# Optimization experiments

Measured on AMD Instinct MI355X. Metric: run time of the kernel, lower is better.

The kernel has to match this reference:

```python
import jax, jax.numpy as jnp
import numpy as np

B, T, N = 128, 32, 196
E = 1024   # embed dim
FD = 1024  # feature dim
H = 1024   # hidden size
A = 1024   # attention dim
SCALE = 0.02


def setup_inputs() -> dict:
    key = jax.random.key(0)
    ks = jax.random.split(key, 16)
    g = lambda k, shape: (jax.random.normal(k, shape, dtype=jnp.float32) * SCALE)
    return {
        "feats": jax.random.normal(ks[0], (B, N, FD), dtype=jnp.float32),
        "embeddings": jax.random.normal(ks[1], (B, T, E), dtype=jnp.float32),
        # additive attention params: v^T tanh(feats @ Wf + h @ Wh + b_att)
        "Wf": g(ks[2], (FD, A)),
        "Wh": g(ks[3], (H, A)),
        "b_att": jnp.zeros((A,), dtype=jnp.float32),
        "v": g(ks[4], (A,)),
        # layer-0 LSTMCell (input = concat(embed, attn) of size E+FD)
        "W_ih0": g(ks[5], (4 * H, E + FD)),
        "W_hh0": g(ks[6], (4 * H, H)),
        "b_ih0": jnp.zeros((4 * H,), dtype=jnp.float32),
        "b_hh0": jnp.zeros((4 * H,), dtype=jnp.float32),
        # layer-1 LSTMCell (input size H)
        "W_ih1": g(ks[7], (4 * H, H)),
        "W_hh1": g(ks[8], (4 * H, H)),
        "b_ih1": jnp.zeros((4 * H,), dtype=jnp.float32),
        "b_hh1": jnp.zeros((4 * H,), dtype=jnp.float32),
    }


def _lstm_cell(x, h, c, W_ih, W_hh, b_ih, b_hh):
    # PyTorch LSTMCell: gates ordered i, f, g, o
    gates = x @ W_ih.T + h @ W_hh.T + (b_ih + b_hh)
    i, f, g, o = jnp.split(gates, 4, axis=-1)
    c_new = jax.nn.sigmoid(f) * c + jax.nn.sigmoid(i) * jnp.tanh(g)
    h_new = jax.nn.sigmoid(o) * jnp.tanh(c_new)
    return h_new, c_new


def reference(feats, embeddings, Wf, Wh, b_att, v, W_ih0, W_hh0, b_ih0, b_hh0,
              W_ih1, W_hh1, b_ih1, b_hh1):
    Bb = embeddings.shape[0]
    # precompute the h-independent half of the attention energies: [B, N, A]
    f_proj = jnp.einsum("bnf,fa->bna", feats, Wf) + b_att

    h0 = jnp.zeros((Bb, H), dtype=feats.dtype)
    c0 = jnp.zeros((Bb, H), dtype=feats.dtype)

    def step(carry, embed_t):
        h0, c0 = carry
        # additive attention with query h0
        e = jnp.tanh(f_proj + (h0 @ Wh)[:, None, :])      # [B, N, A]
        scores = jnp.einsum("bna,a->bn", e, v)            # [B, N]
        alpha = jax.nn.softmax(scores, axis=-1)
        attn = jnp.einsum("bn,bnf->bf", alpha, feats)     # [B, FD]
        x = jnp.concatenate([embed_t, attn], axis=1)      # [B, E+FD]
        h0n, c0n = _lstm_cell(x, h0, c0, W_ih0, W_hh0, b_ih0, b_hh0)
        # faithful to source: layer 1 uses (h0n, c0n) as its state AND h0n as input
        h1, c1 = _lstm_cell(h0n, h0n, c0n, W_ih1, W_hh1, b_ih1, b_hh1)
        return (h0n, c0n), h1

    (_, _), outs = jax.lax.scan(step, (h0, c0), jnp.swapaxes(embeddings, 0, 1))
    return jnp.swapaxes(outs, 0, 1)  # [B, T, H]
```

## Files before the change

kernel.cpp:

```cpp
#include <hip/hip_runtime.h>
#include <cstddef>

typedef unsigned short ushort_t;
typedef unsigned int uint_t;
typedef __attribute__((ext_vector_type(8))) short bf16x8;
typedef __attribute__((ext_vector_type(4))) float f32x4;

constexpr int kB  = 128;
constexpr int kT  = 32;
constexpr int kN  = 196;
constexpr int kH  = 1024;

__device__ __forceinline__ float fsigmoid(float x) { return 1.f / (1.f + __expf(-x)); }
__device__ __forceinline__ float ftanh(float x)    { return 1.f - 2.f / (__expf(2.f * x) + 1.f); }
__device__ __forceinline__ ushort_t f2bf(float f) {
    uint_t u = __float_as_uint(f);
    return (ushort_t)((u + 0x7fffu + ((u >> 16) & 1u)) >> 16);
}

__global__ __launch_bounds__(256) void wf_transpose(
    const float* __restrict__ Wsrc, ushort_t* __restrict__ dst)
{
    __shared__ float t[64][65];
    const int k0 = blockIdx.x * 64, a0 = blockIdx.y * 64;
    const int c = threadIdx.x & 15, r0 = threadIdx.x >> 4;
#pragma unroll
    for (int i = 0; i < 4; ++i) {
        const int r = r0 + i * 16;
        const float4 v = *(const float4*)(Wsrc + (size_t)(k0 + r) * 1024 + a0 + c * 4);
        t[r][c * 4 + 0] = v.x; t[r][c * 4 + 1] = v.y;
        t[r][c * 4 + 2] = v.z; t[r][c * 4 + 3] = v.w;
    }
    __syncthreads();
#pragma unroll
    for (int i = 0; i < 4; ++i) {
        const int r = r0 + i * 16;
        ushort4 h;
        h.x = f2bf(t[c * 4 + 0][r]); h.y = f2bf(t[c * 4 + 1][r]);
        h.z = f2bf(t[c * 4 + 2][r]); h.w = f2bf(t[c * 4 + 3][r]);
        *(ushort4*)&dst[(size_t)(a0 + r) * 1024 + k0 + c * 4] = h;
    }
}

__global__ __launch_bounds__(256) void pack_whh0(
    const float* __restrict__ Whh0, ushort_t* __restrict__ Wbig)
{
    const int idx = blockIdx.x * 256 + threadIdx.x;
    const int j = idx >> 8, k4 = (idx & 255) * 4;
    const int u = j >> 2, g = j & 3;
    const float4 v = *(const float4*)(Whh0 + (size_t)(g * 1024 + u) * 1024 + k4);
    ushort4 h;
    h.x = f2bf(v.x); h.y = f2bf(v.y); h.z = f2bf(v.z); h.w = f2bf(v.w);
    *(ushort4*)&Wbig[(size_t)(1024 + j) * 1024 + k4] = h;
}

__global__ __launch_bounds__(256) void pack_w1sum(
    const float* __restrict__ Wih1, const float* __restrict__ Whh1,
    ushort_t* __restrict__ Wbig)
{
    const int idx = blockIdx.x * 256 + threadIdx.x;
    const int j = idx >> 8, k4 = (idx & 255) * 4;
    const int u = j >> 2, g = j & 3;
    const size_t o = (size_t)(g * 1024 + u) * 1024 + k4;
    const float4 a = *(const float4*)(Wih1 + o);
    const float4 b = *(const float4*)(Whh1 + o);
    ushort4 h;
    h.x = f2bf(a.x + b.x); h.y = f2bf(a.y + b.y);
    h.z = f2bf(a.z + b.z); h.w = f2bf(a.w + b.w);
    *(ushort4*)&Wbig[(size_t)(5120 + j) * 1024 + k4] = h;
}

__global__ __launch_bounds__(256) void pack_w0cat(
    const float* __restrict__ Wih0, ushort_t* __restrict__ W0cat)
{
    const int idx = blockIdx.x * 256 + threadIdx.x;
    const int j = idx >> 9, k4 = (idx & 511) * 4;
    const int u = j >> 2, g = j & 3;
    const int srccol = (k4 < 1024) ? (k4 + 1024) : (k4 - 1024);
    const float4 v = *(const float4*)(Wih0 + (size_t)(g * 1024 + u) * 2048 + srccol);
    ushort4 h;
    h.x = f2bf(v.x); h.y = f2bf(v.y); h.z = f2bf(v.z); h.w = f2bf(v.w);
    *(ushort4*)&W0cat[(size_t)j * 2048 + k4] = h;
}

__global__ __launch_bounds__(256) void cast_bf(
    const float* __restrict__ src, ushort_t* __restrict__ dst)
{
    const size_t idx = ((size_t)blockIdx.x * 256 + threadIdx.x) * 4;
    const float4 v = *(const float4*)(src + idx);
    ushort4 h;
    h.x = f2bf(v.x); h.y = f2bf(v.y); h.z = f2bf(v.z); h.w = f2bf(v.w);
    *(ushort4*)&dst[idx] = h;
}

__global__ __launch_bounds__(256) void fproj_mfma(
    const float* __restrict__ feats, const ushort_t* __restrict__ WfT,
    const float* __restrict__ bias, ushort_t* __restrict__ fprojbf)
{
    __shared__ ushort_t As[128 * 40];
    __shared__ ushort_t Bs[128 * 40];

    const int tid = threadIdx.x;
    const int m0 = blockIdx.x * 128, n0 = blockIdx.y * 128;
    const int lane = tid & 63, w = tid >> 6;
    const int wm = (w & 1) * 64, wn = (w >> 1) * 64;
    const int lr = lane & 15, quad = lane >> 4;

    f32x4 acc[4][4];
#pragma unroll
    for (int i = 0; i < 4; ++i)
#pragma unroll
        for (int j = 0; j < 4; ++j)
            acc[i][j] = (f32x4){0.f, 0.f, 0.f, 0.f};

    for (int k0 = 0; k0 < 1024; k0 += 32) {
#pragma unroll
        for (int it = 0; it < 4; ++it) {
            const int q = it * 256 + tid;
            const int row = q >> 3, kc = (q & 7) * 4;
            const float4 v = *(const float4*)(feats + (size_t)(m0 + row) * 1024 + k0 + kc);
            ushort4 h;
            h.x = f2bf(v.x); h.y = f2bf(v.y); h.z = f2bf(v.z); h.w = f2bf(v.w);
            *(ushort4*)&As[row * 40 + kc] = h;
        }
#pragma unroll
        for (int it = 0; it < 2; ++it) {
            const int q = it * 256 + tid;
            const int row = q >> 2, kc = (q & 3) * 8;
            const uint4 v = *(const uint4*)(WfT + (size_t)(n0 + row) * 1024 + k0 + kc);
            *(uint4*)&Bs[row * 40 + kc] = v;
        }
        __syncthreads();

        bf16x8 af[4], bb[4];
#pragma unroll
        for (int mf = 0; mf < 4; ++mf)
            af[mf] = *(const bf16x8*)&As[(wm + mf * 16 + lr) * 40 + quad * 8];
#pragma unroll
        for (int nf = 0; nf < 4; ++nf)
            bb[nf] = *(const bf16x8*)&Bs[(wn + nf * 16 + lr) * 40 + quad * 8];
#pragma unroll
        for (int mf = 0; mf < 4; ++mf)
#pragma unroll
            for (int nf = 0; nf < 4; ++nf)
                acc[mf][nf] = __builtin_amdgcn_mfma_f32_16x16x32_bf16(
                    af[mf], bb[nf], acc[mf][nf], 0, 0, 0);
        __syncthreads();
    }

#pragma unroll
    for (int nf = 0; nf < 4; ++nf) {
        const int n = n0 + wn + nf * 16 + lr;
        const float bn = bias[n];
#pragma unroll
        for (int mf = 0; mf < 4; ++mf) {
#pragma unroll
            for (int r = 0; r < 4; ++r) {
                const int m = m0 + wm + mf * 16 + quad * 4 + r;
                fprojbf[(size_t)m * 1024 + n] = f2bf(acc[mf][nf][r] + bn);
            }
        }
    }
}

__global__ __launch_bounds__(256) void hgemm_A(
    const ushort_t* __restrict__ hbf, const ushort_t* __restrict__ Wbig,
    const float* __restrict__ cbuf,
    const float* __restrict__ bih1, const float* __restrict__ bhh1,
    float* __restrict__ hwh, float* __restrict__ Ypart,
    float* __restrict__ out, int tstep)
{
    __shared__ ushort_t xs[128 * 40];
    __shared__ ushort_t wsB[64 * 40];
    __shared__ float eps[128][65];

    const int tid = threadIdx.x;
    const int n0 = blockIdx.x * 64;
    const int lane = tid & 63, w = tid >> 6;
    const int wm = (w & 1) * 64, wn = (w >> 1) * 32;
    const int lr = lane & 15, quad = lane >> 4;

    f32x4 acc[4][2];
#pragma unroll
    for (int i = 0; i < 4; ++i) {
        acc[i][0] = (f32x4){0.f, 0.f, 0.f, 0.f};
        acc[i][1] = (f32x4){0.f, 0.f, 0.f, 0.f};
    }

    for (int k0 = 0; k0 < 1024; k0 += 32) {
#pragma unroll
        for (int it = 0; it < 2; ++it) {
            const int q = it * 256 + tid;
            const int row = q >> 2, kc = (q & 3) * 8;
            *(uint4*)&xs[row * 40 + kc] =
                *(const uint4*)&hbf[(size_t)row * 1024 + k0 + kc];
        }
        {
            const int row = tid >> 2, kc = (tid & 3) * 8;
            *(uint4*)&wsB[row * 40 + kc] =
                *(const uint4*)&Wbig[(size_t)(n0 + row) * 1024 + k0 + kc];
        }
        __syncthreads();
        bf16x8 af[4], bb[2];
#pragma unroll
        for (int mf = 0; mf < 4; ++mf)
            af[mf] = *(const bf16x8*)&xs[(wm + mf * 16 + lr) * 40 + quad * 8];
#pragma unroll
        for (int nf = 0; nf < 2; ++nf)
            bb[nf] = *(const bf16x8*)&wsB[(wn + nf * 16 + lr) * 40 + quad * 8];
#pragma unroll
        for (int mf = 0; mf < 4; ++mf)
#pragma unroll
            for (int nf = 0; nf < 2; ++nf)
                acc[mf][nf] = __builtin_amdgcn_mfma_f32_16x16x32_bf16(
                    af[mf], bb[nf], acc[mf][nf], 0, 0, 0);
        __syncthreads();
    }

    if (n0 < 5120) {
        float* dst = (n0 < 1024) ? hwh : Ypart;
        const int stride = (n0 < 1024) ? 1024 : 4096;
        const int nbase = (n0 < 1024) ? n0 : (n0 - 1024);
#pragma unroll
        for (int mf = 0; mf < 4; ++mf)
#pragma unroll
            for (int nf = 0; nf < 2; ++nf)
#pragma unroll
                for (int r = 0; r < 4; ++r) {
                    const int m = wm + mf * 16 + quad * 4 + r;
                    const int n = nbase + wn + nf * 16 + lr;
                    dst[(size_t)m * stride + n] = acc[mf][nf][r];
                }
    } else {
#pragma unroll
        for (int mf = 0; mf < 4; ++mf)
#pragma unroll
            for (int nf = 0; nf < 2; ++nf)
#pragma unroll
                for (int r = 0; r < 4; ++r)
                    eps[wm + mf * 16 + quad * 4 + r][wn + nf * 16 + lr] = acc[mf][nf][r];
        __syncthreads();
        if (tstep >= 1) {
#pragma unroll
            for (int i = 0; i < 8; ++i) {
                const int cid = i * 256 + tid;
                const int b = cid & 127, ulc = cid >> 7;
                const int u = ((n0 - 5120) >> 2) + ulc;
                const float iv = fsigmoid(eps[b][ulc * 4 + 0] + bih1[u]        + bhh1[u]);
                const float fv = fsigmoid(eps[b][ulc * 4 + 1] + bih1[1024 + u] + bhh1[1024 + u]);
                const float gv = ftanh   (eps[b][ulc * 4 + 2] + bih1[2048 + u] + bhh1[2048 + u]);
                const float ov = fsigmoid(eps[b][ulc * 4 + 3] + bih1[3072 + u] + bhh1[3072 + u]);
                const float cp = cbuf[(size_t)b * 1024 + u];
                const float cn = fv * cp + iv * gv;
                out[((size_t)b * kT + (tstep - 1)) * 1024 + u] = ov * ftanh(cn);
            }
        }
    }
}

__global__ __launch_bounds__(256) void scores_kernel(
    const ushort_t* __restrict__ fprojbf, const float* __restrict__ hwh,
    const float* __restrict__ vvec, float* __restrict__ scoresbuf)
{
    const int b = blockIdx.x, chunk = blockIdx.y;
    const int tid = threadIdx.x, lane = tid & 63, w = tid >> 6;

    float hw[16], vr[16];
    {
        const int a0 = lane * 16;
#pragma unroll
        for (int q = 0; q < 4; ++q) {
            const float4 s0 = *(const float4*)(hwh + (size_t)b * 1024 + a0 + q * 4);
            hw[q * 4 + 0] = s0.x; hw[q * 4 + 1] = s0.y;
            hw[q * 4 + 2] = s0.z; hw[q * 4 + 3] = s0.w;
            const float4 vv = *(const float4*)(vvec + a0 + q * 4);
            vr[q * 4 + 0] = vv.x; vr[q * 4 + 1] = vv.y;
            vr[q * 4 + 2] = vv.z; vr[q * 4 + 3] = vv.w;
        }
    }

#pragma unroll
    for (int i = 0; i < 7; ++i) {
        const int n = chunk * 28 + w * 7 + i;
        const ushort_t* fp = fprojbf + ((size_t)(b * kN + n)) * 1024 + lane * 16;
        const uint4 u0 = *(const uint4*)(fp);
        const uint4 u1 = *(const uint4*)(fp + 8);
        float p = 0.f;
        const uint_t uu[8] = {u0.x, u0.y, u0.z, u0.w, u1.x, u1.y, u1.z, u1.w};
#pragma unroll
        for (int q = 0; q < 8; ++q) {
            const float xa = __uint_as_float(uu[q] << 16);
            const float xb = __uint_as_float(uu[q] & 0xffff0000u);
            p += ftanh(xa + hw[2 * q]) * vr[2 * q];
            p += ftanh(xb + hw[2 * q + 1]) * vr[2 * q + 1];
        }
#pragma unroll
        for (int off = 32; off; off >>= 1) p += __shfl_down(p, off);
        if (lane == 0) scoresbuf[b * kN + n] = p;
    }
}

template<int BF>
__global__ __launch_bounds__(256) void attn_kernel(
    const float* __restrict__ scoresbuf, const float* __restrict__ featsf,
    const ushort_t* __restrict__ featsbf, ushort_t* __restrict__ attnbf)
{
    __shared__ float alpha_s[200];
    __shared__ float red[8];
    const int b = blockIdx.x;
    const int tid = threadIdx.x;

    const float val = (tid < kN) ? scoresbuf[b * kN + tid] : -1e30f;
    float m = val;
#pragma unroll
    for (int off = 32; off; off >>= 1) m = fmaxf(m, __shfl_down(m, off));
    if ((tid & 63) == 0) red[tid >> 6] = m;
    __syncthreads();
    m = fmaxf(fmaxf(red[0], red[1]), fmaxf(red[2], red[3]));
    const float e = (tid < kN) ? __expf(val - m) : 0.f;
    float s = e;
#pragma unroll
    for (int off = 32; off; off >>= 1) s += __shfl_down(s, off);
    if ((tid & 63) == 0) red[4 + (tid >> 6)] = s;
    __syncthreads();
    s = red[4] + red[5] + red[6] + red[7];
    if (tid < kN) alpha_s[tid] = e * (1.f / s);
    __syncthreads();

    if (BF) {
        const int f0 = blockIdx.y * 512 + tid * 2;
        const ushort_t* fb = featsbf + (size_t)b * kN * 1024 + f0;
        float a0 = 0.f, a1 = 0.f;
#pragma unroll 4
        for (int n = 0; n < kN; ++n) {
            const uint_t u = *(const uint_t*)(fb + (size_t)n * 1024);
            a0 += alpha_s[n] * __uint_as_float(u << 16);
            a1 += alpha_s[n] * __uint_as_float(u & 0xffff0000u);
        }
        uint_t o = ((uint_t)f2bf(a1) << 16) | (uint_t)f2bf(a0);
        *(uint_t*)&attnbf[(size_t)b * 1024 + f0] = o;
    } else {
        const int f = blockIdx.y * 256 + tid;
        const float* fb = featsf + (size_t)b * kN * 1024 + f;
        float a = 0.f;
#pragma unroll 4
        for (int n = 0; n < kN; ++n) a += alpha_s[n] * fb[(size_t)n * 1024];
        attnbf[(size_t)b * 1024 + f] = f2bf(a);
    }
}

__global__ __launch_bounds__(256) void gatesC(
    const ushort_t* __restrict__ attnbf, const ushort_t* __restrict__ embbf,
    const ushort_t* __restrict__ W0cat, const float* __restrict__ Ypart,
    const float* __restrict__ bih0, const float* __restrict__ bhh0,
    float* __restrict__ cbuf, ushort_t* __restrict__ hbf, int tstep)
{
    __shared__ ushort_t xs[128 * 40];
    __shared__ ushort_t wsB[64 * 40];
    __shared__ float eps[128][65];

    const int tid = threadIdx.x;
    const int n0 = blockIdx.x * 64;
    const int lane = tid & 63, w = tid >> 6;
    const int wm = (w & 1) * 64, wn = (w >> 1) * 32;
    const int lr = lane & 15, quad = lane >> 4;

    f32x4 acc[4][2];
#pragma unroll
    for (int i = 0; i < 4; ++i) {
        acc[i][0] = (f32x4){0.f, 0.f, 0.f, 0.f};
        acc[i][1] = (f32x4){0.f, 0.f, 0.f, 0.f};
    }

    for (int k0 = 0; k0 < 2048; k0 += 32) {
#pragma unroll
        for (int it = 0; it < 2; ++it) {
            const int q = it * 256 + tid;
            const int row = q >> 2, kc = (q & 3) * 8;
            const ushort_t* src = (k0 < 1024)
                ? (attnbf + (size_t)row * 1024 + k0 + kc)
                : (embbf + ((size_t)row * kT + tstep) * 1024 + (k0 - 1024) + kc);
            *(uint4*)&xs[row * 40 + kc] = *(const uint4*)src;
        }
        {
            const int row = tid >> 2, kc = (tid & 3) * 8;
            *(uint4*)&wsB[row * 40 + kc] =
                *(const uint4*)&W0cat[(size_t)(n0 + row) * 2048 + k0 + kc];
        }
        __syncthreads();
        bf16x8 af[4], bb[2];
#pragma unroll
        for (int mf = 0; mf < 4; ++mf)
            af[mf] = *(const bf16x8*)&xs[(wm + mf * 16 + lr) * 40 + quad * 8];
#pragma unroll
        for (int nf = 0; nf < 2; ++nf)
            bb[nf] = *(const bf16x8*)&wsB[(wn + nf * 16 + lr) * 40 + quad * 8];
#pragma unroll
        for (int mf = 0; mf < 4; ++mf)
#pragma unroll
            for (int nf = 0; nf < 2; ++nf)
                acc[mf][nf] = __builtin_amdgcn_mfma_f32_16x16x32_bf16(
                    af[mf], bb[nf], acc[mf][nf], 0, 0, 0);
        __syncthreads();
    }

#pragma unroll
    for (int mf = 0; mf < 4; ++mf)
#pragma unroll
        for (int nf = 0; nf < 2; ++nf)
#pragma unroll
            for (int r = 0; r < 4; ++r)
                eps[wm + mf * 16 + quad * 4 + r][wn + nf * 16 + lr] = acc[mf][nf][r];
    __syncthreads();

#pragma unroll
    for (int i = 0; i < 8; ++i) {
        const int cid = i * 256 + tid;
        const int b = cid & 127, ulc = cid >> 7;
        const int u = (n0 >> 2) + ulc;
        const int jb = n0 + ulc * 4;
        const float* yp = Ypart + (size_t)b * 4096 + jb;
        const float iv = fsigmoid(eps[b][ulc * 4 + 0] + yp[0] + bih0[u]        + bhh0[u]);
        const float fv = fsigmoid(eps[b][ulc * 4 + 1] + yp[1] + bih0[1024 + u] + bhh0[1024 + u]);
        const float gv = ftanh   (eps[b][ulc * 4 + 2] + yp[2] + bih0[2048 + u] + bhh0[2048 + u]);
        const float ov = fsigmoid(eps[b][ulc * 4 + 3] + yp[3] + bih0[3072 + u] + bhh0[3072 + u]);
        const float cp = cbuf[(size_t)b * 1024 + u];
        const float cn = fv * cp + iv * gv;
        cbuf[(size_t)b * 1024 + u] = cn;
        hbf[(size_t)b * 1024 + u] = f2bf(ov * ftanh(cn));
    }
}

extern "C" void kernel_launch(void* const* d_in, const int* in_sizes, int n_in,
                              void* d_out, int out_size, void* d_ws, size_t ws_size,
                              hipStream_t stream)
{
    const float* feats = (const float*)d_in[0];
    const float* emb   = (const float*)d_in[1];
    const float* Wf    = (const float*)d_in[2];
    const float* Wh    = (const float*)d_in[3];
    const float* b_att = (const float*)d_in[4];
    const float* vvec  = (const float*)d_in[5];
    const float* Wih0  = (const float*)d_in[6];
    const float* Whh0  = (const float*)d_in[7];
    const float* bih0  = (const float*)d_in[8];
    const float* bhh0  = (const float*)d_in[9];
    const float* Wih1  = (const float*)d_in[10];
    const float* Whh1  = (const float*)d_in[11];
    const float* bih1  = (const float*)d_in[12];
    const float* bhh1  = (const float*)d_in[13];
    float* out = (float*)d_out;

    ushort_t* fprojbf = (ushort_t*)d_ws;
    ushort_t* embbf   = fprojbf + (size_t)25088 * 1024;
    ushort_t* Wbig    = embbf   + (size_t)4096 * 1024;
    ushort_t* W0cat   = Wbig    + (size_t)9216 * 1024;
    ushort_t* WfT     = W0cat   + (size_t)4096 * 2048;
    ushort_t* hbf     = WfT     + (size_t)1024 * 1024;
    ushort_t* attnbf  = hbf     + (size_t)128 * 1024;
    float* hwh        = (float*)(attnbf + (size_t)128 * 1024);
    float* Ypart      = hwh   + (size_t)128 * 1024;
    float* cbuf       = Ypart + (size_t)128 * 4096;
    float* scoresbuf  = cbuf  + (size_t)128 * 1024;
    ushort_t* featsbf = (ushort_t*)(scoresbuf + 128 * 196);

    const size_t need_full = 152668160;
    const bool use_bf = (ws_size >= need_full);

    hipMemsetAsync(hbf, 0, sizeof(ushort_t) * 128 * 1024, stream);
    hipMemsetAsync(cbuf, 0, sizeof(float) * 128 * 1024, stream);

    wf_transpose<<<dim3(16, 16), 256, 0, stream>>>(Wf, WfT);
    wf_transpose<<<dim3(16, 16), 256, 0, stream>>>(Wh, Wbig);
    pack_whh0<<<4096, 256, 0, stream>>>(Whh0, Wbig);
    pack_w1sum<<<4096, 256, 0, stream>>>(Wih1, Whh1, Wbig);
    pack_w0cat<<<8192, 256, 0, stream>>>(Wih0, W0cat);
    cast_bf<<<4096, 256, 0, stream>>>(emb, embbf);
    if (use_bf) cast_bf<<<25088, 256, 0, stream>>>(feats, featsbf);

    fproj_mfma<<<dim3(196, 8), 256, 0, stream>>>(feats, WfT, b_att, fprojbf);

    for (int t = 0; t < kT; ++t) {
        hgemm_A<<<144, 256, 0, stream>>>(hbf, Wbig, cbuf, bih1, bhh1,
                                         hwh, Ypart, out, t);
        scores_kernel<<<dim3(128, 7), 256, 0, stream>>>(fprojbf, hwh, vvec, scoresbuf);
        if (use_bf)
            attn_kernel<1><<<dim3(128, 2), 256, 0, stream>>>(scoresbuf, feats, featsbf, attnbf);
        else
            attn_kernel<0><<<dim3(128, 4), 256, 0, stream>>>(scoresbuf, feats, featsbf, attnbf);
        gatesC<<<64, 256, 0, stream>>>(attnbf, embbf, W0cat, Ypart,
                                       bih0, bhh0, cbuf, hbf, t);
    }
    hgemm_A<<<144, 256, 0, stream>>>(hbf, Wbig, cbuf, bih1, bhh1,
                                     hwh, Ypart, out, kT);

    (void)in_sizes; (void)n_in; (void)out_size; (void)ws_size;
}
```

Measured before the change: 3.673 ms.

## Double-buffer LDS tiles in GEMM kernels, widen gatesC grid, use bf16 feats in fproj

```diff
diff --git a/kernel.cpp b/kernel.cpp
--- a/kernel.cpp
+++ b/kernel.cpp
@@ -93,19 +93,24 @@
     *(ushort4*)&dst[idx] = h;
 }
 
+template<int BF>
 __global__ __launch_bounds__(256) void fproj_mfma(
-    const float* __restrict__ feats, const ushort_t* __restrict__ WfT,
+    const float* __restrict__ featsf, const ushort_t* __restrict__ featsbf,
+    const ushort_t* __restrict__ WfT,
     const float* __restrict__ bias, ushort_t* __restrict__ fprojbf)
 {
-    __shared__ ushort_t As[128 * 40];
-    __shared__ ushort_t Bs[128 * 40];
+    __shared__ ushort_t As[2][128 * 40];
+    __shared__ ushort_t Bs[2][128 * 40];
 
     const int tid = threadIdx.x;
-    const int m0 = blockIdx.x * 128, n0 = blockIdx.y * 128;
+    const int n0 = blockIdx.x * 128, m0 = blockIdx.y * 128;
     const int lane = tid & 63, w = tid >> 6;
     const int wm = (w & 1) * 64, wn = (w >> 1) * 64;
     const int lr = lane & 15, quad = lane >> 4;
 
+    const int xrow0 = tid >> 2, xrow1 = 64 + (tid >> 2);
+    const int xkc = (tid & 3) * 8;
+
     f32x4 acc[4][4];
 #pragma unroll
     for (int i = 0; i < 4; ++i)
@@ -113,39 +118,62 @@
         for (int j = 0; j < 4; ++j)
             acc[i][j] = (f32x4){0.f, 0.f, 0.f, 0.f};
 
-    for (int k0 = 0; k0 < 1024; k0 += 32) {
-#pragma unroll
-        for (int it = 0; it < 4; ++it) {
-            const int q = it * 256 + tid;
-            const int row = q >> 3, kc = (q & 7) * 4;
-            const float4 v = *(const float4*)(feats + (size_t)(m0 + row) * 1024 + k0 + kc);
+    uint4 a0r, a1r, b0r, b1r;
+    float4 f00, f01, f10, f11;
+
+    auto LOAD = [&](int k0) {
+        if (BF) {
+            a0r = *(const uint4*)&featsbf[(size_t)(m0 + xrow0) * 1024 + k0 + xkc];
+            a1r = *(const uint4*)&featsbf[(size_t)(m0 + xrow1) * 1024 + k0 + xkc];
+        } else {
+            f00 = *(const float4*)&featsf[(size_t)(m0 + xrow0) * 1024 + k0 + xkc];
+            f01 = *(const float4*)&featsf[(size_t)(m0 + xrow0) * 1024 + k0 + xkc + 4];
+            f10 = *(const float4*)&featsf[(size_t)(m0 + xrow1) * 1024 + k0 + xkc];
+            f11 = *(const float4*)&featsf[(size_t)(m0 + xrow1) * 1024 + k0 + xkc + 4];
+        }
+        b0r = *(const uint4*)&WfT[(size_t)(n0 + xrow0) * 1024 + k0 + xkc];
+        b1r = *(const uint4*)&WfT[(size_t)(n0 + xrow1) * 1024 + k0 + xkc];
+    };
+    auto WRITE = [&](int buf) {
+        if (BF) {
+            *(uint4*)&As[buf][xrow0 * 40 + xkc] = a0r;
+            *(uint4*)&As[buf][xrow1 * 40 + xkc] = a1r;
+        } else {
             ushort4 h;
-            h.x = f2bf(v.x); h.y = f2bf(v.y); h.z = f2bf(v.z); h.w = f2bf(v.w);
-            *(ushort4*)&As[row * 40 + kc] = h;
-        }
-#pragma unroll
-        for (int it = 0; it < 2; ++it) {
-            const int q = it * 256 + tid;
-            const int row = q >> 2, kc = (q & 3) * 8;
-            const uint4 v = *(const uint4*)(WfT + (size_t)(n0 + row) * 1024 + k0 + kc);
-            *(uint4*)&Bs[row * 40 + kc] = v;
-        }
-        __syncthreads();
-
+            h.x = f2bf(f00.x); h.y = f2bf(f00.y); h.z = f2bf(f00.z); h.w = f2bf(f00.w);
+            *(ushort4*)&As[buf][xrow0 * 40 + xkc] = h;
+            h.x = f2bf(f01.x); h.y = f2bf(f01.y); h.z = f2bf(f01.z); h.w = f2bf(f01.w);
+            *(ushort4*)&As[buf][xrow0 * 40 + xkc + 4] = h;
+            h.x = f2bf(f10.x); h.y = f2bf(f10.y); h.z = f2bf(f10.z); h.w = f2bf(f10.w);
+            *(ushort4*)&As[buf][xrow1 * 40 + xkc] = h;
+            h.x = f2bf(f11.x); h.y = f2bf(f11.y); h.z = f2bf(f11.z); h.w = f2bf(f11.w);
+            *(ushort4*)&As[buf][xrow1 * 40 + xkc + 4] = h;
+        }
+        *(uint4*)&Bs[buf][xrow0 * 40 + xkc] = b0r;
+        *(uint4*)&Bs[buf][xrow1 * 40 + xkc] = b1r;
+    };
+
+    LOAD(0); WRITE(0); __syncthreads();
+    int cur = 0;
+    for (int k0 = 32; k0 <= 1024; k0 += 32) {
+        const bool more = (k0 < 1024);
+        if (more) LOAD(k0);
         bf16x8 af[4], bb[4];
 #pragma unroll
         for (int mf = 0; mf < 4; ++mf)
-            af[mf] = *(const bf16x8*)&As[(wm + mf * 16 + lr) * 40 + quad * 8];
+            af[mf] = *(const bf16x8*)&As[cur][(wm + mf * 16 + lr) * 40 + quad * 8];
 #pragma unroll
         for (int nf = 0; nf < 4; ++nf)
-            bb[nf] = *(const bf16x8*)&Bs[(wn + nf * 16 + lr) * 40 + quad * 8];
+            bb[nf] = *(const bf16x8*)&Bs[cur][(wn + nf * 16 + lr) * 40 + quad * 8];
 #pragma unroll
         for (int mf = 0; mf < 4; ++mf)
 #pragma unroll
             for (int nf = 0; nf < 4; ++nf)
                 acc[mf][nf] = __builtin_amdgcn_mfma_f32_16x16x32_bf16(
                     af[mf], bb[nf], acc[mf][nf], 0, 0, 0);
+        if (more) WRITE(cur ^ 1);
         __syncthreads();
+        cur ^= 1;
     }
 
 #pragma unroll
@@ -170,8 +198,8 @@
     float* __restrict__ hwh, float* __restrict__ Ypart,
     float* __restrict__ out, int tstep)
 {
-    __shared__ ushort_t xs[128 * 40];
-    __shared__ ushort_t wsB[64 * 40];
+    __shared__ ushort_t xs[2][128 * 40];
+    __shared__ ushort_t wsB[2][64 * 40];
     __shared__ float eps[128][65];
 
     const int tid = threadIdx.x;
@@ -180,6 +208,9 @@
     const int wm = (w & 1) * 64, wn = (w >> 1) * 32;
     const int lr = lane & 15, quad = lane >> 4;
 
+    const int xrow0 = tid >> 2, xrow1 = 64 + (tid >> 2);
+    const int xkc = (tid & 3) * 8;
+
     f32x4 acc[4][2];
 #pragma unroll
     for (int i = 0; i < 4; ++i) {
@@ -187,34 +218,39 @@
         acc[i][1] = (f32x4){0.f, 0.f, 0.f, 0.f};
     }
 
-    for (int k0 = 0; k0 < 1024; k0 += 32) {
-#pragma unroll
-        for (int it = 0; it < 2; ++it) {
-            const int q = it * 256 + tid;
-            const int row = q >> 2, kc = (q & 3) * 8;
-            *(uint4*)&xs[row * 40 + kc] =
-                *(const uint4*)&hbf[(size_t)row * 1024 + k0 + kc];
-        }
-        {
-            const int row = tid >> 2, kc = (tid & 3) * 8;
-            *(uint4*)&wsB[row * 40 + kc] =
-                *(const uint4*)&Wbig[(size_t)(n0 + row) * 1024 + k0 + kc];
-        }
-        __syncthreads();
+    uint4 x0r, x1r, w0r;
+    auto LOAD = [&](int k0) {
+        x0r = *(const uint4*)&hbf[(size_t)xrow0 * 1024 + k0 + xkc];
+        x1r = *(const uint4*)&hbf[(size_t)xrow1 * 1024 + k0 + xkc];
+        w0r = *(const uint4*)&Wbig[(size_t)(n0 + xrow0) * 1024 + k0 + xkc];
+    };
+    auto WRITE = [&](int buf) {
+        *(uint4*)&xs[buf][xrow0 * 40 + xkc] = x0r;
+        *(uint4*)&xs[buf][xrow1 * 40 + xkc] = x1r;
+        *(uint4*)&wsB[buf][xrow0 * 40 + xkc] = w0r;
+    };
+
+    LOAD(0); WRITE(0); __syncthreads();
+    int cur = 0;
+    for (int k0 = 32; k0 <= 1024; k0 += 32) {
+        const bool more = (k0 < 1024);
+        if (more) LOAD(k0);
         bf16x8 af[4], bb[2];
 #pragma unroll
         for (int mf = 0; mf < 4; ++mf)
-            af[mf] = *(const bf16x8*)&xs[(wm + mf * 16 + lr) * 40 + quad * 8];
+            af[mf] = *(const bf16x8*)&xs[cur][(wm + mf * 16 + lr) * 40 + quad * 8];
 #pragma unroll
         for (int nf = 0; nf < 2; ++nf)
-            bb[nf] = *(const bf16x8*)&wsB[(wn + nf * 16 + lr) * 40 + quad * 8];
+            bb[nf] = *(const bf16x8*)&wsB[cur][(wn + nf * 16 + lr) * 40 + quad * 8];
 #pragma unroll
         for (int mf = 0; mf < 4; ++mf)
 #pragma unroll
             for (int nf = 0; nf < 2; ++nf)
                 acc[mf][nf] = __builtin_amdgcn_mfma_f32_16x16x32_bf16(
                     af[mf], bb[nf], acc[mf][nf], 0, 0, 0);
+        if (more) WRITE(cur ^ 1);
         __syncthreads();
+        cur ^= 1;
     }
 
     if (n0 < 5120) {
@@ -355,66 +391,70 @@
     const float* __restrict__ bih0, const float* __restrict__ bhh0,
     float* __restrict__ cbuf, ushort_t* __restrict__ hbf, int tstep)
 {
-    __shared__ ushort_t xs[128 * 40];
-    __shared__ ushort_t wsB[64 * 40];
-    __shared__ float eps[128][65];
+    __shared__ ushort_t xs[2][128 * 40];
+    __shared__ ushort_t ws2[2][32 * 40];
+    __shared__ float eps[128][33];
 
     const int tid = threadIdx.x;
-    const int n0 = blockIdx.x * 64;
+    const int n0 = blockIdx.x * 32;
     const int lane = tid & 63, w = tid >> 6;
-    const int wm = (w & 1) * 64, wn = (w >> 1) * 32;
+    const int wm = (w & 1) * 64, wn = (w >> 1) * 16;
     const int lr = lane & 15, quad = lane >> 4;
 
-    f32x4 acc[4][2];
+    const int xrow0 = tid >> 2, xrow1 = 64 + (tid >> 2);
+    const int xkc = (tid & 3) * 8;
+    const int wrow = tid >> 3, wkc = (tid & 7) * 4;
+
+    f32x4 acc[4];
+#pragma unroll
+    for (int i = 0; i < 4; ++i) acc[i] = (f32x4){0.f, 0.f, 0.f, 0.f};
+
+    uint4 x0r, x1r; uint2 w0r;
+    auto LOAD = [&](int k0) {
+        const ushort_t* s0 = (k0 < 1024)
+            ? (attnbf + (size_t)xrow0 * 1024 + k0)
+            : (embbf + ((size_t)xrow0 * kT + tstep) * 1024 + (k0 - 1024));
+        const ushort_t* s1 = (k0 < 1024)
+            ? (attnbf + (size_t)xrow1 * 1024 + k0)
+            : (embbf + ((size_t)xrow1 * kT + tstep) * 1024 + (k0 - 1024));
+        x0r = *(const uint4*)(s0 + xkc);
+        x1r = *(const uint4*)(s1 + xkc);
+        w0r = *(const uint2*)&W0cat[(size_t)(n0 + wrow) * 2048 + k0 + wkc];
+    };
+    auto WRITE = [&](int buf) {
+        *(uint4*)&xs[buf][xrow0 * 40 + xkc] = x0r;
+        *(uint4*)&xs[buf][xrow1 * 40 + xkc] = x1r;
+        *(uint2*)&ws2[buf][wrow * 40 + wkc] = w0r;
+    };
+
+    LOAD(0); WRITE(0); __syncthreads();
+    int cur = 0;
+    for (int k0 = 32; k0 <= 2048; k0 += 32) {
+        const bool more = (k0 < 2048);
+        if (more) LOAD(k0);
+        bf16x8 af[4], bb;
+#pragma unroll
+        for (int mf = 0; mf < 4; ++mf)
+            af[mf] = *(const bf16x8*)&xs[cur][(wm + mf * 16 + lr) * 40 + quad * 8];
+        bb = *(const bf16x8*)&ws2[cur][(wn + lr) * 40 + quad * 8];
+#pragma unroll
+        for (int mf = 0; mf < 4; ++mf)
+            acc[mf] = __builtin_amdgcn_mfma_f32_16x16x32_bf16(
+                af[mf], bb, acc[mf], 0, 0, 0);
+        if (more) WRITE(cur ^ 1);
+        __syncthreads();
+        cur ^= 1;
+    }
+
+#pragma unroll
+    for (int mf = 0; mf < 4; ++mf)
+#pragma unroll
+        for (int r = 0; r < 4; ++r)
+            eps[wm + mf * 16 + quad * 4 + r][wn + lr] = acc[mf][r];
+    __syncthreads();
+
 #pragma unroll
     for (int i = 0; i < 4; ++i) {
-        acc[i][0] = (f32x4){0.f, 0.f, 0.f, 0.f};
-        acc[i][1] = (f32x4){0.f, 0.f, 0.f, 0.f};
-    }
-
-    for (int k0 = 0; k0 < 2048; k0 += 32) {
-#pragma unroll
-        for (int it = 0; it < 2; ++it) {
-            const int q = it * 256 + tid;
-            const int row = q >> 2, kc = (q & 3) * 8;
-            const ushort_t* src = (k0 < 1024)
-                ? (attnbf + (size_t)row * 1024 + k0 + kc)
-                : (embbf + ((size_t)row * kT + tstep) * 1024 + (k0 - 1024) + kc);
-            *(uint4*)&xs[row * 40 + kc] = *(const uint4*)src;
-        }
-        {
-            const int row = tid >> 2, kc = (tid & 3) * 8;
-            *(uint4*)&wsB[row * 40 + kc] =
-                *(const uint4*)&W0cat[(size_t)(n0 + row) * 2048 + k0 + kc];
-        }
-        __syncthreads();
-        bf16x8 af[4], bb[2];
-#pragma unroll
-        for (int mf = 0; mf < 4; ++mf)
-            af[mf] = *(const bf16x8*)&xs[(wm + mf * 16 + lr) * 40 + quad * 8];
-#pragma unroll
-        for (int nf = 0; nf < 2; ++nf)
-            bb[nf] = *(const bf16x8*)&wsB[(wn + nf * 16 + lr) * 40 + quad * 8];
-#pragma unroll
-        for (int mf = 0; mf < 4; ++mf)
-#pragma unroll
-            for (int nf = 0; nf < 2; ++nf)
-                acc[mf][nf] = __builtin_amdgcn_mfma_f32_16x16x32_bf16(
-                    af[mf], bb[nf], acc[mf][nf], 0, 0, 0);
-        __syncthreads();
-    }
-
-#pragma unroll
-    for (int mf = 0; mf < 4; ++mf)
-#pragma unroll
-        for (int nf = 0; nf < 2; ++nf)
-#pragma unroll
-            for (int r = 0; r < 4; ++r)
-                eps[wm + mf * 16 + quad * 4 + r][wn + nf * 16 + lr] = acc[mf][nf][r];
-    __syncthreads();
-
-#pragma unroll
-    for (int i = 0; i < 8; ++i) {
         const int cid = i * 256 + tid;
         const int b = cid & 127, ulc = cid >> 7;
         const int u = (n0 >> 2) + ulc;
@@ -478,7 +518,10 @@
     cast_bf<<<4096, 256, 0, stream>>>(emb, embbf);
     if (use_bf) cast_bf<<<25088, 256, 0, stream>>>(feats, featsbf);
 
-    fproj_mfma<<<dim3(196, 8), 256, 0, stream>>>(feats, WfT, b_att, fprojbf);
+    if (use_bf)
+        fproj_mfma<1><<<dim3(8, 196), 256, 0, stream>>>(feats, featsbf, WfT, b_att, fprojbf);
+    else
+        fproj_mfma<0><<<dim3(8, 196), 256, 0, stream>>>(feats, featsbf, WfT, b_att, fprojbf);
 
     for (int t = 0; t < kT; ++t) {
         hgemm_A<<<144, 256, 0, stream>>>(hbf, Wbig, cbuf, bih1, bhh1,
@@ -488,8 +531,8 @@
             attn_kernel<1><<<dim3(128, 2), 256, 0, stream>>>(scoresbuf, feats, featsbf, attnbf);
         else
             attn_kernel<0><<<dim3(128, 4), 256, 0, stream>>>(scoresbuf, feats, featsbf, attnbf);
-        gatesC<<<64, 256, 0, stream>>>(attnbf, embbf, W0cat, Ypart,
-                                       bih0, bhh0, cbuf, hbf, t);
+        gatesC<<<128, 256, 0, stream>>>(attnbf, embbf, W0cat, Ypart,
+                                        bih0, bhh0, cbuf, hbf, t);
     }
     hgemm_A<<<144, 256, 0, stream>>>(hbf, Wbig, cbuf, bih1, bhh1,
                                      hwh, Ypart, out, kT);
```

Measured after the change: 3.228 ms. 12.1% less time.
